# Kernel optimization log

Hardware: AMD Instinct MI355X
Metric: run time of the kernel (lower is better)

Reference implementation:

```python
import jax, jax.numpy as jnp
import numpy as np

B, DIM, Hs, Ws_ = 16, 96, 112, 112
HEADS, WS, OUT = 3, 7, 96
DH = OUT // HEADS


def _rel_index(ws):
    ch = np.arange(ws)
    coords = np.stack(np.meshgrid(ch, ch, indexing='ij'), 0).reshape(2, -1)
    rel = (coords[:, :, None] - coords[:, None, :]).transpose(1, 2, 0).copy()
    rel[..., 0] += ws - 1
    rel[..., 1] += ws - 1
    rel[..., 0] *= 2 * ws - 1
    return rel.sum(-1)  # [ws*ws, ws*ws]


def grid_sample_zeros(img, grid):
    # img [N,C,H,W], grid [N,Hg,Wg,2] with (x,y) in [-1,1]; bilinear, align_corners=True, zeros padding
    N, C, H, W = img.shape
    x = (grid[..., 0] + 1.0) * 0.5 * (W - 1)
    y = (grid[..., 1] + 1.0) * 0.5 * (H - 1)
    x0 = jnp.floor(x); y0 = jnp.floor(y)
    x1 = x0 + 1.0; y1 = y0 + 1.0
    wa = (x1 - x) * (y1 - y); wb = (x - x0) * (y1 - y)
    wc = (x1 - x) * (y - y0); wd = (x - x0) * (y - y0)

    def gather(ix, iy):
        valid = ((ix >= 0) & (ix <= W - 1) & (iy >= 0) & (iy <= H - 1)).astype(img.dtype)
        ixc = jnp.clip(ix, 0, W - 1).astype(jnp.int32)
        iyc = jnp.clip(iy, 0, H - 1).astype(jnp.int32)
        vals = jax.vmap(lambda im, yy, xx: im[:, yy, xx])(img, iyc, ixc)  # [N,C,Hg,Wg]
        return vals * valid[:, None, :, :]

    return (gather(x0, y0) * wa[:, None] + gather(x1, y0) * wb[:, None]
            + gather(x0, y1) * wc[:, None] + gather(x1, y1) * wd[:, None])


def setup_inputs() -> dict:
    key = jax.random.key(0)
    ks = jax.random.split(key, 8)
    s = 0.02
    return {
        'x': jax.random.normal(ks[0], (B, DIM, Hs, Ws_), jnp.float32),
        'w_qkv': jax.random.normal(ks[1], (3 * OUT, DIM), jnp.float32) * s,
        'b_qkv': jnp.zeros((3 * OUT,), jnp.float32),
        'w_off': jax.random.normal(ks[2], (2 * HEADS, DIM), jnp.float32) * s,
        'b_off': jnp.zeros((2 * HEADS,), jnp.float32),
        'w_scl': jax.random.normal(ks[3], (2 * HEADS, DIM), jnp.float32) * s,
        'b_scl': jnp.zeros((2 * HEADS,), jnp.float32),
        'rpb': jax.random.normal(ks[4], ((2 * WS - 1) ** 2, HEADS), jnp.float32) * s,
        'w_proj': jax.random.normal(ks[5], (OUT, OUT), jnp.float32) * s,
        'b_proj': jnp.zeros((OUT,), jnp.float32),
    }


def _forward(x, w_qkv, b_qkv, w_off, b_off, w_scl, b_scl, rpb, w_proj, b_proj):
    b, C, h, w = x.shape
    ws, H, dh = WS, HEADS, DH
    scale = (C // H) ** -0.5
    pad_td = (ws - h % ws) % ws; pad_lr = (ws - w % ws) % ws
    pt, pd = pad_td // 2, pad_td - pad_td // 2
    pl, pr = pad_lr // 2, pad_lr - pad_lr // 2
    eh, ew = h + pad_td, w + pad_lr
    wnh, wnw = eh // ws, ew // ws
    xp = jnp.pad(x, ((0, 0), (0, 0), (pt, pd), (pl, pr)))

    # base reference grid, channel 0 = x (width), channel 1 = y (height)
    irh = jnp.linspace(-1.0, 1.0, eh); irw = jnp.linspace(-1.0, 1.0, ew)
    base = jnp.stack([jnp.broadcast_to(irw[None, :], (eh, ew)),
                      jnp.broadcast_to(irh[:, None], (eh, ew))], 0).reshape(2, wnh, ws, wnw, ws)
    bch = jnp.arange(ws) * 2.0 / (eh - 1); bch = bch - bch.mean()
    bcw = jnp.arange(ws) * 2.0 / (ew - 1); bcw = bcw - bcw.mean()
    wc = jnp.stack([jnp.broadcast_to(bcw[None, None, None, :], (wnh, ws, wnw, ws)),
                    jnp.broadcast_to(bch[None, :, None, None], (wnh, ws, wnw, ws))], 0)

    # per-window offset / scale prediction: avgpool(ws) -> leaky_relu -> 1x1 conv
    pooled = xp.reshape(b, C, wnh, ws, wnw, ws).mean(axis=(3, 5))
    act = jax.nn.leaky_relu(pooled)  # slope 0.01, matches torch default
    off = (jnp.einsum('bchw,oc->bohw', act, w_off) + b_off[None, :, None, None]).reshape(b * H, 2, wnh, wnw)
    off = jnp.stack([off[:, 0] / (h // ws), off[:, 1] / (w // ws)], 1)
    scl = (jnp.einsum('bchw,oc->bohw', act, w_scl) + b_scl[None, :, None, None]).reshape(b * H, 2, wnh, wnw)

    coords = base[None] + wc[None] * scl[:, :, :, None, :, None] + off[:, :, :, None, :, None]
    grid = coords.transpose(0, 2, 3, 4, 5, 1).reshape(b * H, eh, ew, 2)

    qkv = jnp.einsum('bchw,oc->bohw', x, w_qkv) + b_qkv[None, :, None, None]
    qkv = qkv.reshape(b, 3, H, dh, h, w).transpose(1, 0, 2, 3, 4, 5).reshape(3 * b * H, dh, h, w)
    qkv = jnp.pad(qkv, ((0, 0), (0, 0), (pt, pd), (pl, pr))).reshape(3, b * H, dh, eh, ew)
    q, k, v = qkv[0], qkv[1], qkv[2]

    k_s = grid_sample_zeros(k, grid)
    v_s = grid_sample_zeros(v, grid)

    def to_win(t):  # [b*H, dh, eh, ew] -> [b*wnh*wnw, H, ws*ws, dh]
        return t.reshape(b, H, dh, wnh, ws, wnw, ws).transpose(0, 3, 5, 1, 4, 6, 2).reshape(b * wnh * wnw, H, ws * ws, dh)

    qw, kw, vw = to_win(q), to_win(k_s), to_win(v_s)
    dots = jnp.einsum('wnqd,wnkd->wnqk', qw, kw) * scale
    rel_idx = jnp.asarray(_rel_index(ws))
    bias = rpb[rel_idx.reshape(-1)].reshape(ws * ws, ws * ws, H).transpose(2, 0, 1)
    attn = jax.nn.softmax(dots + bias[None], axis=-1)
    out = jnp.einsum('wnqk,wnkd->wnqd', attn, vw)
    out = out.reshape(b, wnh, wnw, H, ws, ws, dh).transpose(0, 3, 6, 1, 4, 2, 5).reshape(b, H * dh, eh, ew)
    out = out[:, :, pt:h + pt, pl:w + pl]
    out = jnp.einsum('bchw,oc->bohw', out, w_proj) + b_proj[None, :, None, None]
    return out


def reference(x, w_qkv, b_qkv, w_off, b_off, w_scl, b_scl, rpb, w_proj, b_proj):
    return _forward(x, w_qkv, b_qkv, w_off, b_off, w_scl, b_scl, rpb, w_proj, b_proj)
```

## Files before the change

### kernel.cpp

```cpp
#include <hip/hip_runtime.h>
#include <hip/hip_bf16.h>
#include <stdint.h>

#define NB 16
#define CDIM 96
#define HW 112
#define NPOS (HW*HW)
#define NHEAD 3
#define DH 32
#define WN 16
#define NWIN (WN*WN)
#define SCALE 0.17677669529663687f

typedef __attribute__((ext_vector_type(8))) short bf16x8;
typedef __attribute__((ext_vector_type(4))) float f32x4;

__device__ __forceinline__ float bfbits_lo(uint32_t w){ union{uint32_t u; float f;} a; a.u = w<<16; return a.f; }
__device__ __forceinline__ float bfbits_hi(uint32_t w){ union{uint32_t u; float f;} a; a.u = w & 0xFFFF0000u; return a.f; }
__device__ __forceinline__ uint32_t packbf(float x, float y){
  union{float f; uint32_t u;} a, b; a.f = x; b.f = y;
  uint32_t ua = a.u + 0x7FFFu + ((a.u>>16)&1u);
  uint32_t ub = b.u + 0x7FFFu + ((b.u>>16)&1u);
  return (ua>>16) | (ub & 0xFFFF0000u);
}
__device__ __forceinline__ unsigned short f2bf(float x){
  union{float f; uint32_t u;} a; a.f = x;
  return (unsigned short)((a.u + 0x7FFFu + ((a.u>>16)&1u))>>16);
}

__global__ void k_pool_act(const float* __restrict__ x, float* __restrict__ act){
  int n = blockIdx.x*256 + threadIdx.x;
  int ww = n & 15; int wh = (n>>4)&15; int bc = n>>8;
  const float* src = x + (size_t)bc*NPOS + (size_t)(wh*7)*HW + ww*7;
  float s = 0.f;
  #pragma unroll
  for (int r=0;r<7;r++){
    const float* row = src + r*HW;
    s += row[0]+row[1]+row[2]+row[3]+row[4]+row[5]+row[6];
  }
  s *= (1.f/49.f);
  act[n] = s > 0.f ? s : 0.01f*s;
}

__global__ void k_offscl(const float* __restrict__ act,
                         const float* __restrict__ woff, const float* __restrict__ boff,
                         const float* __restrict__ wscl, const float* __restrict__ bscl,
                         float4* __restrict__ offscl){
  int n = blockIdx.x*256 + threadIdx.x;
  int b = n >> 8; int wpos = n & 255;
  float accO[6], accS[6];
  #pragma unroll
  for (int o=0;o<6;o++){ accO[o]=boff[o]; accS[o]=bscl[o]; }
  const float* a = act + (size_t)b*CDIM*NWIN + wpos;
  for (int c=0;c<CDIM;c++){
    float av = a[(size_t)c*NWIN];
    #pragma unroll
    for (int o=0;o<6;o++){ accO[o] += av*woff[o*CDIM+c]; accS[o] += av*wscl[o*CDIM+c]; }
  }
  #pragma unroll
  for (int h=0;h<NHEAD;h++){
    float4 r;
    r.x = accO[2*h]   * (1.f/16.f);
    r.y = accO[2*h+1] * (1.f/16.f);
    r.z = accS[2*h];
    r.w = accS[2*h+1];
    offscl[(size_t)(b*NHEAD+h)*NWIN + wpos] = r;
  }
}

__global__ void k_bias_pre(const float* __restrict__ rpb, float* __restrict__ bias_g){
  int n = blockIdx.x*256 + threadIdx.x;
  if (n >= 3*64*64) return;
  int h = n >> 12; int q = (n>>6)&63; int k = n&63;
  float v = -1e30f;
  if (k < 49){
    int qc = q < 49 ? q : 48;
    int qi = qc/7, qj = qc - (qc/7)*7;
    int ki = k/7,  kj = k - (k/7)*7;
    v = rpb[((qi-ki+6)*13 + (qj-kj+6))*3 + h];
  }
  bias_g[n] = v;
}

__launch_bounds__(256)
__global__ void k_qkv_mfma(const float* __restrict__ x, const float* __restrict__ wqkv,
                           const float* __restrict__ bqkv,
                           unsigned short* __restrict__ q, unsigned short* __restrict__ kk,
                           unsigned short* __restrict__ v){
  __shared__ float xf[96*72];
  __shared__ uint4 xbf4[64*13];
  __shared__ uint4 wbf4[96*13];
  const int t = threadIdx.x;
  const int b = blockIdx.x / 196;
  const int p0 = (blockIdx.x % 196) * 64;

  #pragma unroll
  for (int i=0;i<6;i++){
    int f = t + i*256; int c = f>>4; int p4 = (f&15)*4;
    *(float4*)(xf + c*72 + p4) = *(const float4*)(x + (size_t)(b*CDIM+c)*NPOS + p0 + p4);
  }
  __syncthreads();
  #pragma unroll
  for (int i=0;i<3;i++){
    int u = t + i*256; int pos = u & 63; int oct = u >> 6;
    uint32_t pk0 = packbf(xf[(oct*8+0)*72+pos], xf[(oct*8+1)*72+pos]);
    uint32_t pk1 = packbf(xf[(oct*8+2)*72+pos], xf[(oct*8+3)*72+pos]);
    uint32_t pk2 = packbf(xf[(oct*8+4)*72+pos], xf[(oct*8+5)*72+pos]);
    uint32_t pk3 = packbf(xf[(oct*8+6)*72+pos], xf[(oct*8+7)*72+pos]);
    xbf4[pos*13 + oct] = make_uint4(pk0,pk1,pk2,pk3);
  }

  const int lane = t & 63, wv = t >> 6;
  const int g = lane >> 4, r16 = lane & 15;
  const int pos = p0 + wv*16 + r16;

  for (int s=0;s<3;s++){
    if (s) __syncthreads();
    #pragma unroll
    for (int i=0;i<9;i++){
      int f = t + i*256; int o = f/24; int c4m = f%24;
      float4 wvv = *(const float4*)(wqkv + (size_t)(s*96+o)*CDIM + c4m*4);
      ((uint2*)wbf4)[o*26 + c4m] = make_uint2(packbf(wvv.x,wvv.y), packbf(wvv.z,wvv.w));
    }
    __syncthreads();

    f32x4 acc[6];
    #pragma unroll
    for (int nf=0;nf<6;nf++) acc[nf] = (f32x4){0.f,0.f,0.f,0.f};
    #pragma unroll
    for (int ks=0;ks<3;ks++){
      bf16x8 xb = *(const bf16x8*)&xbf4[(wv*16 + r16)*13 + ks*4 + g];
      #pragma unroll
      for (int nf=0;nf<6;nf++){
        bf16x8 wf = *(const bf16x8*)&wbf4[(nf*16 + r16)*13 + ks*4 + g];
        acc[nf] = __builtin_amdgcn_mfma_f32_16x16x32_bf16(wf, xb, acc[nf], 0,0,0);
      }
    }
    unsigned short* dst = (s==0)?q:((s==1)?kk:v);
    float sc = (s==0) ? SCALE : 1.f;
    #pragma unroll
    for (int nf=0;nf<6;nf++){
      int o0 = nf*16 + 4*g;
      int hh = o0 >> 5; int d0 = o0 & 31;
      float4 bv = *(const float4*)(bqkv + s*96 + o0);
      uint2 pk = make_uint2(packbf((acc[nf][0]+bv.x)*sc, (acc[nf][1]+bv.y)*sc),
                            packbf((acc[nf][2]+bv.z)*sc, (acc[nf][3]+bv.w)*sc));
      *(uint2*)(dst + ((size_t)(b*NHEAD+hh)*NPOS + pos)*DH + d0) = pk;
    }
  }
}

__launch_bounds__(128)
__global__ void k_attn_mfma(const unsigned short* __restrict__ qb,
                            const unsigned short* __restrict__ kb,
                            const unsigned short* __restrict__ vb,
                            const float4* __restrict__ offscl,
                            const float* __restrict__ bias_g,
                            float* __restrict__ aout){
  __shared__ unsigned short VT_all[2*2048];
  const int h   = blockIdx.x % 3;
  const int grp = blockIdx.x / 3;
  const int wv  = threadIdx.x >> 6;
  const int lane = threadIdx.x & 63;
  const int win = grp*2 + wv;
  const int b = win>>8, wh=(win>>4)&15, ww=win&15;
  const int bh = b*NHEAD + h;
  const int g = lane>>4, r16 = lane&15;
  unsigned short* VT_s = VT_all + wv*2048;

  uint4 qf[4];
  #pragma unroll
  for (int qt=0;qt<4;qt++){
    int qq = qt*16 + r16; if (qq > 48) qq = 48;
    int qi = qq/7; int qj = qq - qi*7;
    size_t pos = (size_t)(wh*7+qi)*HW + ww*7 + qj;
    qf[qt] = *(const uint4*)(qb + ((size_t)bh*NPOS + pos)*DH + g*8);
  }

  int ki = lane/7; int kj = lane - ki*7;
  uint32_t nbaddr[4]; float nbw[4];
  {
    float4 os = offscl[(size_t)bh*NWIN + (wh*16+ww)];
    float px = (float)(ww*7+kj) + (float)(kj-3)*os.z + 55.5f*os.x;
    float py = (float)(wh*7+ki) + (float)(ki-3)*os.w + 55.5f*os.y;
    float x0f = floorf(px), y0f = floorf(py);
    float fx = px-x0f, fy = py-y0f;
    int x0 = (int)x0f, y0 = (int)y0f;
    float wb[4] = {(1.f-fx)*(1.f-fy), fx*(1.f-fy), (1.f-fx)*fy, fx*fy};
    bool qok = lane < 49;
    #pragma unroll
    for (int nb=0;nb<4;nb++){
      int xi = x0 + (nb&1), yi = y0 + (nb>>1);
      int xc = min(max(xi,0),HW-1), yc = min(max(yi,0),HW-1);
      nbaddr[nb] = (uint32_t)(yc*HW + xc) * 64u;
      nbw[nb] = (qok && xi==xc && yi==yc) ? wb[nb] : 0.f;
    }
  }

  const char* kb8 = (const char*)kb + (size_t)bh*NPOS*64;
  const char* vb8 = (const char*)vb + (size_t)bh*NPOS*64;
  uint4 kfrag[4];
  #pragma unroll
  for (int pp=0;pp<4;pp++){
    int spos = pp*16 + r16;
    float ka[8], va[8];
    #pragma unroll
    for (int j=0;j<8;j++){ ka[j]=0.f; va[j]=0.f; }
    #pragma unroll
    for (int nb=0;nb<4;nb++){
      uint32_t a = (uint32_t)__shfl((int)nbaddr[nb], spos);
      float    w = __shfl(nbw[nb], spos);
      uint4 uk = *(const uint4*)(kb8 + a + g*16);
      uint4 uv = *(const uint4*)(vb8 + a + g*16);
      ka[0]+=w*bfbits_lo(uk.x); ka[1]+=w*bfbits_hi(uk.x);
      ka[2]+=w*bfbits_lo(uk.y); ka[3]+=w*bfbits_hi(uk.y);
      ka[4]+=w*bfbits_lo(uk.z); ka[5]+=w*bfbits_hi(uk.z);
      ka[6]+=w*bfbits_lo(uk.w); ka[7]+=w*bfbits_hi(uk.w);
      va[0]+=w*bfbits_lo(uv.x); va[1]+=w*bfbits_hi(uv.x);
      va[2]+=w*bfbits_lo(uv.y); va[3]+=w*bfbits_hi(uv.y);
      va[4]+=w*bfbits_lo(uv.z); va[5]+=w*bfbits_hi(uv.z);
      va[6]+=w*bfbits_lo(uv.w); va[7]+=w*bfbits_hi(uv.w);
    }
    kfrag[pp] = make_uint4(packbf(ka[0],ka[1]), packbf(ka[2],ka[3]),
                           packbf(ka[4],ka[5]), packbf(ka[6],ka[7]));
    #pragma unroll
    for (int j=0;j<8;j++){
      int d = g*8 + j;
      VT_s[d*64 + (((spos>>3) ^ (d&7))*8) + (spos&7)] = f2bf(va[j]);
    }
  }

  __builtin_amdgcn_sched_barrier(0);
  __syncthreads();
  __builtin_amdgcn_sched_barrier(0);

  const float* bias_h = bias_g + h*4096;
  f32x4 acc[4][4];
  #pragma unroll
  for (int qt=0;qt<4;qt++){
    int qq = qt*16 + r16;
    #pragma unroll
    for (int at=0;at<4;at++)
      acc[at][qt] = *(const f32x4*)(bias_h + qq*64 + at*16 + g*4);
  }
  #pragma unroll
  for (int at=0;at<4;at++){
    bf16x8 a = *(const bf16x8*)&kfrag[at];
    #pragma unroll
    for (int qt=0;qt<4;qt++)
      acc[at][qt] = __builtin_amdgcn_mfma_f32_16x16x32_bf16(a, *(const bf16x8*)&qf[qt], acc[at][qt], 0,0,0);
  }

  #pragma unroll
  for (int qt=0;qt<4;qt++){
    float m = acc[0][qt][0];
    #pragma unroll
    for (int at=0;at<4;at++)
      #pragma unroll
      for (int rr=0;rr<4;rr++) m = fmaxf(m, acc[at][qt][rr]);
    m = fmaxf(m, __shfl_xor(m, 16));
    m = fmaxf(m, __shfl_xor(m, 32));
    float s = 0.f;
    #pragma unroll
    for (int at=0;at<4;at++)
      #pragma unroll
      for (int rr=0;rr<4;rr++){ float e = __expf(acc[at][qt][rr]-m); acc[at][qt][rr]=e; s+=e; }
    s += __shfl_xor(s, 16);
    s += __shfl_xor(s, 32);
    float rl = 1.f/s;
    #pragma unroll
    for (int at=0;at<4;at++)
      #pragma unroll
      for (int rr=0;rr<4;rr++) acc[at][qt][rr] *= rl;
  }

  uint32_t plo[4][4], phi[4][4];
  #pragma unroll
  for (int at=0;at<4;at++)
    #pragma unroll
    for (int qt=0;qt<4;qt++){
      plo[at][qt] = packbf(acc[at][qt][0], acc[at][qt][1]);
      phi[at][qt] = packbf(acc[at][qt][2], acc[at][qt][3]);
    }

  f32x4 o[2][4];
  #pragma unroll
  for (int dt=0;dt<2;dt++)
    #pragma unroll
    for (int qt=0;qt<4;qt++) o[dt][qt] = (f32x4){0.f,0.f,0.f,0.f};

  #pragma unroll
  for (int kt=0;kt<2;kt++){
    uint4 pfrag[4];
    const int s0 = ((2*g)&3)*16 + r16;
    const int s1 = ((2*g+1)&3)*16 + r16;
    const bool odd = (g & 2);
    #pragma unroll
    for (int qt=0;qt<4;qt++){
      uint32_t e_lo0 = (uint32_t)__shfl((int)plo[2*kt  ][qt], s0);
      uint32_t e_hi0 = (uint32_t)__shfl((int)phi[2*kt  ][qt], s0);
      uint32_t e_lo1 = (uint32_t)__shfl((int)plo[2*kt  ][qt], s1);
      uint32_t e_hi1 = (uint32_t)__shfl((int)phi[2*kt  ][qt], s1);
      uint32_t o_lo0 = (uint32_t)__shfl((int)plo[2*kt+1][qt], s0);
      uint32_t o_hi0 = (uint32_t)__shfl((int)phi[2*kt+1][qt], s0);
      uint32_t o_lo1 = (uint32_t)__shfl((int)plo[2*kt+1][qt], s1);
      uint32_t o_hi1 = (uint32_t)__shfl((int)phi[2*kt+1][qt], s1);
      pfrag[qt] = make_uint4(odd?o_lo0:e_lo0, odd?o_hi0:e_hi0,
                             odd?o_lo1:e_lo1, odd?o_hi1:e_hi1);
    }
    #pragma unroll
    for (int dt=0;dt<2;dt++){
      int d = dt*16 + r16;
      bf16x8 a = *(const bf16x8*)&VT_s[d*64 + (((kt*4+g) ^ (d&7))*8)];
      #pragma unroll
      for (int qt=0;qt<4;qt++)
        o[dt][qt] = __builtin_amdgcn_mfma_f32_16x16x32_bf16(a, *(const bf16x8*)&pfrag[qt], o[dt][qt], 0,0,0);
    }
  }

  float* outb = aout + ((size_t)b*CDIM + h*DH)*NPOS;
  #pragma unroll
  for (int qt=0;qt<4;qt++){
    int q = qt*16 + r16;
    if (q < 49){
      int qi = q/7; int qj = q - qi*7;
      size_t opix = (size_t)(wh*7+qi)*HW + ww*7 + qj;
      #pragma unroll
      for (int dt=0;dt<2;dt++)
        #pragma unroll
        for (int rr=0;rr<4;rr++){
          int d = dt*16 + g*4 + rr;
          outb[(size_t)d*NPOS + opix] = o[dt][qt][rr];
        }
    }
  }
}

__launch_bounds__(256)
__global__ void k_proj_mfma(const float* yin, const float* __restrict__ wproj,
                            const float* __restrict__ bproj, float* yout){
  __shared__ float xf[96*72];
  __shared__ uint4 xbf4[64*13];
  __shared__ uint4 wbf4[96*13];
  const int t = threadIdx.x;
  const int b = blockIdx.x / 196;
  const int p0 = (blockIdx.x % 196) * 64;

  #pragma unroll
  for (int i=0;i<6;i++){
    int f = t + i*256; int c = f>>4; int p4 = (f&15)*4;
    *(float4*)(xf + c*72 + p4) = *(const float4*)(yin + (size_t)(b*CDIM+c)*NPOS + p0 + p4);
  }
  __syncthreads();
  #pragma unroll
  for (int i=0;i<3;i++){
    int u = t + i*256; int pos = u & 63; int oct = u >> 6;
    uint32_t pk0 = packbf(xf[(oct*8+0)*72+pos], xf[(oct*8+1)*72+pos]);
    uint32_t pk1 = packbf(xf[(oct*8+2)*72+pos], xf[(oct*8+3)*72+pos]);
    uint32_t pk2 = packbf(xf[(oct*8+4)*72+pos], xf[(oct*8+5)*72+pos]);
    uint32_t pk3 = packbf(xf[(oct*8+6)*72+pos], xf[(oct*8+7)*72+pos]);
    xbf4[pos*13 + oct] = make_uint4(pk0,pk1,pk2,pk3);
  }
  #pragma unroll
  for (int i=0;i<9;i++){
    int f = t + i*256; int o = f/24; int c4m = f%24;
    float4 wvv = *(const float4*)(wproj + (size_t)o*CDIM + c4m*4);
    ((uint2*)wbf4)[o*26 + c4m] = make_uint2(packbf(wvv.x,wvv.y), packbf(wvv.z,wvv.w));
  }
  __syncthreads();

  const int lane = t & 63, wv = t >> 6;
  const int g = lane >> 4, r16 = lane & 15;
  const int pos = p0 + wv*16 + r16;
  f32x4 acc[6];
  #pragma unroll
  for (int nf=0;nf<6;nf++) acc[nf] = (f32x4){0.f,0.f,0.f,0.f};
  #pragma unroll
  for (int ks=0;ks<3;ks++){
    bf16x8 xb = *(const bf16x8*)&xbf4[(wv*16 + r16)*13 + ks*4 + g];
    #pragma unroll
    for (int nf=0;nf<6;nf++){
      bf16x8 wf = *(const bf16x8*)&wbf4[(nf*16 + r16)*13 + ks*4 + g];
      acc[nf] = __builtin_amdgcn_mfma_f32_16x16x32_bf16(wf, xb, acc[nf], 0,0,0);
    }
  }
  #pragma unroll
  for (int nf=0;nf<6;nf++){
    int o0 = nf*16 + 4*g;
    float4 bv = *(const float4*)(bproj + o0);
    yout[(size_t)(b*CDIM+o0+0)*NPOS + pos] = acc[nf][0] + bv.x;
    yout[(size_t)(b*CDIM+o0+1)*NPOS + pos] = acc[nf][1] + bv.y;
    yout[(size_t)(b*CDIM+o0+2)*NPOS + pos] = acc[nf][2] + bv.z;
    yout[(size_t)(b*CDIM+o0+3)*NPOS + pos] = acc[nf][3] + bv.w;
  }
}

extern "C" void kernel_launch(void* const* d_in, const int* in_sizes, int n_in,
                              void* d_out, int out_size, void* d_ws, size_t ws_size,
                              hipStream_t stream) {
  const float* x      = (const float*)d_in[0];
  const float* w_qkv  = (const float*)d_in[1];
  const float* b_qkv  = (const float*)d_in[2];
  const float* w_off  = (const float*)d_in[3];
  const float* b_off  = (const float*)d_in[4];
  const float* w_scl  = (const float*)d_in[5];
  const float* b_scl  = (const float*)d_in[6];
  const float* rpb    = (const float*)d_in[7];
  const float* w_proj = (const float*)d_in[8];
  const float* b_proj = (const float*)d_in[9];

  char* ws = (char*)d_ws;
  float*   act    = (float*)(ws + 0);
  float4*  offscl = (float4*)(ws + 1572864);
  float*   bias_g = (float*)(ws + 1769472);
  const size_t QKV_BYTES = (size_t)NB*NHEAD*NPOS*DH*2;
  unsigned short* qbuf = (unsigned short*)(ws + 2097152);
  unsigned short* kbuf = (unsigned short*)(ws + 2097152 + QKV_BYTES);
  unsigned short* vbuf = (unsigned short*)(ws + 2097152 + 2*QKV_BYTES);

  hipLaunchKernelGGL(k_pool_act,  dim3(1536), dim3(256), 0, stream, x, act);
  hipLaunchKernelGGL(k_offscl,    dim3(16),   dim3(256), 0, stream, act, w_off, b_off, w_scl, b_scl, offscl);
  hipLaunchKernelGGL(k_bias_pre,  dim3(48),   dim3(256), 0, stream, rpb, bias_g);
  hipLaunchKernelGGL(k_qkv_mfma,  dim3(16*196), dim3(256), 0, stream, x, w_qkv, b_qkv, qbuf, kbuf, vbuf);
  hipLaunchKernelGGL(k_attn_mfma, dim3(3*2048), dim3(128), 0, stream,
                     qbuf, kbuf, vbuf, offscl, bias_g, (float*)d_out);
  hipLaunchKernelGGL(k_proj_mfma, dim3(16*196), dim3(256), 0, stream,
                     (const float*)d_out, w_proj, b_proj, (float*)d_out);
}
```

Baseline: 205.8 us.

## Pre-convert weights to bf16 once and load MFMA fragments directly from global

Adds a small kernel that converts the qkv and projection weights to bf16 once per call. The qkv and proj GEMM kernels now drop their shared-memory staging: each lane loads its activation fragment straight from global memory (strided per channel) and packs it in registers, and weight fragments are read directly from the bf16 global buffer. This removes the per-block fp32 weight conversion, the LDS round trips and most barriers, at the cost of uncoalesced strided activation loads and repeated weight reads served from cache. A barrier is added in proj before the in-place write to keep read-before-write ordering within the block.

```diff
diff --git a/kernel.cpp b/kernel.cpp
--- a/kernel.cpp
+++ b/kernel.cpp
@@ -26,6 +26,13 @@
 __device__ __forceinline__ unsigned short f2bf(float x){
   union{float f; uint32_t u;} a; a.f = x;
   return (unsigned short)((a.u + 0x7FFFu + ((a.u>>16)&1u))>>16);
+}
+
+__global__ void k_wpre(const float* __restrict__ wqkv, const float* __restrict__ wproj,
+                       unsigned short* __restrict__ w16q, unsigned short* __restrict__ w16p){
+  int n = blockIdx.x*256 + threadIdx.x;
+  if (n < 288*96) w16q[n] = f2bf(wqkv[n]);
+  if (n < 96*96)  w16p[n] = f2bf(wproj[n]);
 }
 
 __global__ void k_pool_act(const float* __restrict__ x, float* __restrict__ act){
@@ -83,57 +90,41 @@
 }
 
 __launch_bounds__(256)
-__global__ void k_qkv_mfma(const float* __restrict__ x, const float* __restrict__ wqkv,
+__global__ void k_qkv_mfma(const float* __restrict__ x, const unsigned short* __restrict__ w16,
                            const float* __restrict__ bqkv,
                            unsigned short* __restrict__ q, unsigned short* __restrict__ kk,
                            unsigned short* __restrict__ v){
-  __shared__ float xf[96*72];
-  __shared__ uint4 xbf4[64*13];
-  __shared__ uint4 wbf4[96*13];
   const int t = threadIdx.x;
   const int b = blockIdx.x / 196;
   const int p0 = (blockIdx.x % 196) * 64;
-
-  #pragma unroll
-  for (int i=0;i<6;i++){
-    int f = t + i*256; int c = f>>4; int p4 = (f&15)*4;
-    *(float4*)(xf + c*72 + p4) = *(const float4*)(x + (size_t)(b*CDIM+c)*NPOS + p0 + p4);
-  }
-  __syncthreads();
-  #pragma unroll
-  for (int i=0;i<3;i++){
-    int u = t + i*256; int pos = u & 63; int oct = u >> 6;
-    uint32_t pk0 = packbf(xf[(oct*8+0)*72+pos], xf[(oct*8+1)*72+pos]);
-    uint32_t pk1 = packbf(xf[(oct*8+2)*72+pos], xf[(oct*8+3)*72+pos]);
-    uint32_t pk2 = packbf(xf[(oct*8+4)*72+pos], xf[(oct*8+5)*72+pos]);
-    uint32_t pk3 = packbf(xf[(oct*8+6)*72+pos], xf[(oct*8+7)*72+pos]);
-    xbf4[pos*13 + oct] = make_uint4(pk0,pk1,pk2,pk3);
-  }
-
   const int lane = t & 63, wv = t >> 6;
   const int g = lane >> 4, r16 = lane & 15;
   const int pos = p0 + wv*16 + r16;
 
+  uint4 afu[3];
+  {
+    const float* xb = x + (size_t)b*CDIM*NPOS + pos;
+    #pragma unroll
+    for (int ks=0;ks<3;ks++){
+      float xv[8];
+      #pragma unroll
+      for (int j=0;j<8;j++) xv[j] = xb[(size_t)(ks*32 + 8*g + j)*NPOS];
+      afu[ks] = make_uint4(packbf(xv[0],xv[1]), packbf(xv[2],xv[3]),
+                           packbf(xv[4],xv[5]), packbf(xv[6],xv[7]));
+    }
+  }
+
   for (int s=0;s<3;s++){
-    if (s) __syncthreads();
-    #pragma unroll
-    for (int i=0;i<9;i++){
-      int f = t + i*256; int o = f/24; int c4m = f%24;
-      float4 wvv = *(const float4*)(wqkv + (size_t)(s*96+o)*CDIM + c4m*4);
-      ((uint2*)wbf4)[o*26 + c4m] = make_uint2(packbf(wvv.x,wvv.y), packbf(wvv.z,wvv.w));
-    }
-    __syncthreads();
-
     f32x4 acc[6];
     #pragma unroll
     for (int nf=0;nf<6;nf++) acc[nf] = (f32x4){0.f,0.f,0.f,0.f};
     #pragma unroll
     for (int ks=0;ks<3;ks++){
-      bf16x8 xb = *(const bf16x8*)&xbf4[(wv*16 + r16)*13 + ks*4 + g];
       #pragma unroll
       for (int nf=0;nf<6;nf++){
-        bf16x8 wf = *(const bf16x8*)&wbf4[(nf*16 + r16)*13 + ks*4 + g];
-        acc[nf] = __builtin_amdgcn_mfma_f32_16x16x32_bf16(wf, xb, acc[nf], 0,0,0);
+        uint4 wu = *(const uint4*)(w16 + ((size_t)(s*96 + nf*16 + r16)*96 + ks*32 + 8*g));
+        acc[nf] = __builtin_amdgcn_mfma_f32_16x16x32_bf16(*(const bf16x8*)&wu,
+                                                          *(const bf16x8*)&afu[ks], acc[nf], 0,0,0);
       }
     }
     unsigned short* dst = (s==0)?q:((s==1)?kk:v);
@@ -337,53 +328,43 @@
 }
 
 __launch_bounds__(256)
-__global__ void k_proj_mfma(const float* yin, const float* __restrict__ wproj,
+__global__ void k_proj_mfma(const float* yin, const unsigned short* __restrict__ w16,
                             const float* __restrict__ bproj, float* yout){
-  __shared__ float xf[96*72];
-  __shared__ uint4 xbf4[64*13];
-  __shared__ uint4 wbf4[96*13];
   const int t = threadIdx.x;
   const int b = blockIdx.x / 196;
   const int p0 = (blockIdx.x % 196) * 64;
-
-  #pragma unroll
-  for (int i=0;i<6;i++){
-    int f = t + i*256; int c = f>>4; int p4 = (f&15)*4;
-    *(float4*)(xf + c*72 + p4) = *(const float4*)(yin + (size_t)(b*CDIM+c)*NPOS + p0 + p4);
-  }
-  __syncthreads();
-  #pragma unroll
-  for (int i=0;i<3;i++){
-    int u = t + i*256; int pos = u & 63; int oct = u >> 6;
-    uint32_t pk0 = packbf(xf[(oct*8+0)*72+pos], xf[(oct*8+1)*72+pos]);
-    uint32_t pk1 = packbf(xf[(oct*8+2)*72+pos], xf[(oct*8+3)*72+pos]);
-    uint32_t pk2 = packbf(xf[(oct*8+4)*72+pos], xf[(oct*8+5)*72+pos]);
-    uint32_t pk3 = packbf(xf[(oct*8+6)*72+pos], xf[(oct*8+7)*72+pos]);
-    xbf4[pos*13 + oct] = make_uint4(pk0,pk1,pk2,pk3);
-  }
-  #pragma unroll
-  for (int i=0;i<9;i++){
-    int f = t + i*256; int o = f/24; int c4m = f%24;
-    float4 wvv = *(const float4*)(wproj + (size_t)o*CDIM + c4m*4);
-    ((uint2*)wbf4)[o*26 + c4m] = make_uint2(packbf(wvv.x,wvv.y), packbf(wvv.z,wvv.w));
-  }
-  __syncthreads();
-
   const int lane = t & 63, wv = t >> 6;
   const int g = lane >> 4, r16 = lane & 15;
   const int pos = p0 + wv*16 + r16;
+
+  uint4 afu[3];
+  {
+    const float* xb = yin + (size_t)b*CDIM*NPOS + pos;
+    #pragma unroll
+    for (int ks=0;ks<3;ks++){
+      float xv[8];
+      #pragma unroll
+      for (int j=0;j<8;j++) xv[j] = xb[(size_t)(ks*32 + 8*g + j)*NPOS];
+      afu[ks] = make_uint4(packbf(xv[0],xv[1]), packbf(xv[2],xv[3]),
+                           packbf(xv[4],xv[5]), packbf(xv[6],xv[7]));
+    }
+  }
+
   f32x4 acc[6];
   #pragma unroll
   for (int nf=0;nf<6;nf++) acc[nf] = (f32x4){0.f,0.f,0.f,0.f};
   #pragma unroll
   for (int ks=0;ks<3;ks++){
-    bf16x8 xb = *(const bf16x8*)&xbf4[(wv*16 + r16)*13 + ks*4 + g];
     #pragma unroll
     for (int nf=0;nf<6;nf++){
-      bf16x8 wf = *(const bf16x8*)&wbf4[(nf*16 + r16)*13 + ks*4 + g];
-      acc[nf] = __builtin_amdgcn_mfma_f32_16x16x32_bf16(wf, xb, acc[nf], 0,0,0);
-    }
-  }
+      uint4 wu = *(const uint4*)(w16 + ((size_t)(nf*16 + r16)*96 + ks*32 + 8*g));
+      acc[nf] = __builtin_amdgcn_mfma_f32_16x16x32_bf16(*(const bf16x8*)&wu,
+                                                        *(const bf16x8*)&afu[ks], acc[nf], 0,0,0);
+    }
+  }
+
+  __syncthreads();
+
   #pragma unroll
   for (int nf=0;nf<6;nf++){
     int o0 = nf*16 + 4*g;
@@ -413,17 +394,20 @@
   float*   act    = (float*)(ws + 0);
   float4*  offscl = (float4*)(ws + 1572864);
   float*   bias_g = (float*)(ws + 1769472);
+  unsigned short* w16q = (unsigned short*)(ws + 1818624);
+  unsigned short* w16p = (unsigned short*)(ws + 1873920);
   const size_t QKV_BYTES = (size_t)NB*NHEAD*NPOS*DH*2;
   unsigned short* qbuf = (unsigned short*)(ws + 2097152);
   unsigned short* kbuf = (unsigned short*)(ws + 2097152 + QKV_BYTES);
   unsigned short* vbuf = (unsigned short*)(ws + 2097152 + 2*QKV_BYTES);
 
+  hipLaunchKernelGGL(k_wpre,      dim3(108),  dim3(256), 0, stream, w_qkv, w_proj, w16q, w16p);
   hipLaunchKernelGGL(k_pool_act,  dim3(1536), dim3(256), 0, stream, x, act);
   hipLaunchKernelGGL(k_offscl,    dim3(16),   dim3(256), 0, stream, act, w_off, b_off, w_scl, b_scl, offscl);
   hipLaunchKernelGGL(k_bias_pre,  dim3(48),   dim3(256), 0, stream, rpb, bias_g);
-  hipLaunchKernelGGL(k_qkv_mfma,  dim3(16*196), dim3(256), 0, stream, x, w_qkv, b_qkv, qbuf, kbuf, vbuf);
+  hipLaunchKernelGGL(k_qkv_mfma,  dim3(16*196), dim3(256), 0, stream, x, w16q, b_qkv, qbuf, kbuf, vbuf);
   hipLaunchKernelGGL(k_attn_mfma, dim3(3*2048), dim3(128), 0, stream,
                      qbuf, kbuf, vbuf, offscl, bias_g, (float*)d_out);
   hipLaunchKernelGGL(k_proj_mfma, dim3(16*196), dim3(256), 0, stream,
-                     (const float*)d_out, w_proj, b_proj, (float*)d_out);
-}
+                     (const float*)d_out, w16p, b_proj, (float*)d_out);
+}
```

Measured after the change: 243.0 us. 18.0% more time.
